# Kernel tuning notes

Measured on AMD Instinct MI355X. Metric: run time of the kernel, lower is better.

The kernel has to match this reference:

```python
import jax, jax.numpy as jnp
import numpy as np

R = 16
LORA_ALPHA = 16.0
SCALING = LORA_ALPHA / R  # = 1.0, matches lora_alpha / r


def setup_inputs() -> dict:
    key = jax.random.key(0)
    k_x, k_a, k_a0, k_b = jax.random.split(key, 4)
    d, r, n_tok = 4096, R, 8192
    inv_sqrt_d = 1.0 / np.sqrt(d)
    x = jax.random.normal(k_x, (n_tok, d), dtype=jnp.float32)
    # mode='standard': A0 ~ N(0, 1/d), B0 = 0; A, B initialized as clones of A0, B0
    A0 = jax.random.normal(k_a0, (r, d), dtype=jnp.float32) * inv_sqrt_d
    B0 = jnp.zeros((d, r), dtype=jnp.float32)
    # perturb A, B slightly to emulate trained params (still faithful math)
    A = A0 + jax.random.normal(k_a, (r, d), dtype=jnp.float32) * inv_sqrt_d
    B = B0 + jax.random.normal(k_b, (d, r), dtype=jnp.float32) * inv_sqrt_d
    return {"x": x, "A": A, "B": B, "A0": A0, "B0": B0}


def reference(x, A, B, A0, B0):
    # Faithful to torch: dW = (B @ A - B0 @ A0) * scaling; out = x @ dW
    # (mode='standard' uses the offset-subtracted delta)
    dW = (B @ A - B0 @ A0) * SCALING          # [d, d]
    return x @ dW                              # [N, d]
```

## Files before the change

### kernel.cpp

```cpp
#include <hip/hip_runtime.h>

#define N_TOK 8192
#define D     4096
#define RLO   16
#define R2    32

typedef __bf16  bf16x8  __attribute__((ext_vector_type(8)));
typedef short   short8v __attribute__((ext_vector_type(8)));
typedef float   f32x4   __attribute__((ext_vector_type(4)));

__device__ __forceinline__ short bf1(float f) {
  __bf16 b = (__bf16)f;
  return __builtin_bit_cast(short, b);
}

__device__ __forceinline__ short8v cvt8(float4 lo, float4 hi) {
  bf16x8 b;
  b[0] = (__bf16)lo.x; b[1] = (__bf16)lo.y; b[2] = (__bf16)lo.z; b[3] = (__bf16)lo.w;
  b[4] = (__bf16)hi.x; b[5] = (__bf16)hi.y; b[6] = (__bf16)hi.z; b[7] = (__bf16)hi.w;
  return __builtin_bit_cast(short8v, b);
}


__global__ __launch_bounds__(256) void prep_kernel(
    const float* __restrict__ A, const float* __restrict__ B,
    const float* __restrict__ A0, const float* __restrict__ B0,
    ushort* __restrict__ PTb, ushort* __restrict__ Qpk) {
  int idx = blockIdx.x * 256 + threadIdx.x;
  int r = idx >> 12;
  int k = idx & (D - 1);
  float pt, q;
  if (r < RLO) {
    pt = B[k * RLO + r];
    q  = A[r * D + k];
  } else {
    pt = -B0[k * RLO + (r - RLO)];
    q  = A0[(r - RLO) * D + k];
  }
  PTb[idx] = (ushort)bf1(pt);
  Qpk[(size_t)k * R2 + r] = (ushort)bf1(q);
}

__global__ __launch_bounds__(256) void fused_kernel(
    const float* __restrict__ x, const ushort* __restrict__ PTb,
    const ushort* __restrict__ Qpk, float* __restrict__ out) {
  __shared__ float red[4][16][R2 + 2];
  __shared__ __align__(16) ushort usb[16][R2];
  const int tid  = threadIdx.x;
  const int w    = tid >> 6;
  const int lane = tid & 63;
  const int l16  = lane & 15;
  const int kg   = lane >> 4;
  const int row0 = blockIdx.x * 16;
  const int kb   = w * 1024 + kg * 8;

  const float*  xp  = x   + (size_t)(row0 + l16) * D + kb;
  const ushort* pb0 = PTb + (size_t)l16 * D + kb;
  const ushort* pb1 = pb0 + (size_t)16 * D;

  f32x4 acc0 = {0.f, 0.f, 0.f, 0.f};
  f32x4 acc1 = {0.f, 0.f, 0.f, 0.f};

#pragma unroll
  for (int s = 0; s < 32; ++s) {
    const int ko = s * 32;
    const float4 alo = *(const float4*)(xp + ko);
    const float4 ahi = *(const float4*)(xp + ko + 4);
    const short8v b0 = *(const short8v*)(pb0 + ko);
    const short8v b1 = *(const short8v*)(pb1 + ko);
    const short8v a  = cvt8(alo, ahi);
    acc0 = __builtin_amdgcn_mfma_f32_16x16x32_bf16(a, b0, acc0, 0, 0, 0);
    acc1 = __builtin_amdgcn_mfma_f32_16x16x32_bf16(a, b1, acc1, 0, 0, 0);
  }

#pragma unroll
  for (int j = 0; j < 4; ++j) {
    red[w][kg * 4 + j][l16]      = acc0[j];
    red[w][kg * 4 + j][16 + l16] = acc1[j];
  }
  __syncthreads();

#pragma unroll
  for (int half = 0; half < 2; ++half) {
    const int idx = half * 256 + tid;
    const int row = idx >> 5;
    const int r   = idx & 31;
    const float s = red[0][row][r] + red[1][row][r] +
                    red[2][row][r] + red[3][row][r];
    usb[row][r] = (ushort)bf1(s);
  }
  __syncthreads();

  const short8v ua = *(const short8v*)&usb[l16][kg * 8];
  const f32x4 z = {0.f, 0.f, 0.f, 0.f};
  const int jbase = w * 1024;

#pragma unroll 8
  for (int jt = 0; jt < 64; ++jt) {
    const int j = jbase + jt * 16 + l16;
    const short8v qb = *(const short8v*)(Qpk + (size_t)j * R2 + kg * 8);
    const f32x4 d = __builtin_amdgcn_mfma_f32_16x16x32_bf16(ua, qb, z, 0, 0, 0);
    float* o = out + (size_t)(row0 + kg * 4) * D + j;
#pragma unroll
    for (int jr = 0; jr < 4; ++jr)
      __builtin_nontemporal_store(d[jr], o + (size_t)jr * D);
  }
}

extern "C" void kernel_launch(void* const* d_in, const int* in_sizes, int n_in,
                              void* d_out, int out_size, void* d_ws, size_t ws_size,
                              hipStream_t stream) {
  const float* x  = (const float*)d_in[0];
  const float* A  = (const float*)d_in[1];
  const float* B  = (const float*)d_in[2];
  const float* A0 = (const float*)d_in[3];
  const float* B0 = (const float*)d_in[4];
  float* out = (float*)d_out;

  ushort* PTb = (ushort*)d_ws;
  ushort* Qpk = PTb + (size_t)R2 * D;

  hipLaunchKernelGGL(prep_kernel, dim3((R2 * D) / 256), dim3(256), 0, stream,
                     A, B, A0, B0, PTb, Qpk);
  hipLaunchKernelGGL(fused_kernel, dim3(N_TOK / 16), dim3(256), 0, stream,
                     x, PTb, Qpk, out);
}
```

Before: 64.38 us.

## Split fused LoRA kernel into split-K projection and separate expansion kernel

Breaks the single fused kernel into two launches. The first computes x·[B,-B0] partial sums with the K dimension split four ways, using four times as many blocks, and writes fp32 partials to workspace. The second sums the partials and runs the rank-32 expansion that writes the output. The aim is to overlap the x read phase and the output write phase across many more blocks, at the cost of an extra launch and a small round trip of the partials through global memory.

New measurement: 93.05 us. 1.45x slower.

```diff
diff --git a/kernel.cpp b/kernel.cpp
--- a/kernel.cpp
+++ b/kernel.cpp
@@ -4,6 +4,7 @@
 #define D     4096
 #define RLO   16
 #define R2    32
+#define KS    4
 
 typedef __bf16  bf16x8  __attribute__((ext_vector_type(8)));
 typedef short   short8v __attribute__((ext_vector_type(8)));
@@ -41,18 +42,19 @@
   Qpk[(size_t)k * R2 + r] = (ushort)bf1(q);
 }
 
-__global__ __launch_bounds__(256) void fused_kernel(
+__global__ __launch_bounds__(256) void s1_kernel(
     const float* __restrict__ x, const ushort* __restrict__ PTb,
-    const ushort* __restrict__ Qpk, float* __restrict__ out) {
+    float* __restrict__ UP) {
   __shared__ float red[4][16][R2 + 2];
-  __shared__ __align__(16) ushort usb[16][R2];
   const int tid  = threadIdx.x;
   const int w    = tid >> 6;
   const int lane = tid & 63;
   const int l16  = lane & 15;
   const int kg   = lane >> 4;
-  const int row0 = blockIdx.x * 16;
-  const int kb   = w * 1024 + kg * 8;
+  const int rowblk = (int)blockIdx.x >> 2;
+  const int ks     = blockIdx.x & 3;
+  const int row0 = rowblk * 16;
+  const int kb   = ks * 1024 + w * 256 + kg * 8;
 
   const float*  xp  = x   + (size_t)(row0 + l16) * D + kb;
   const ushort* pb0 = PTb + (size_t)l16 * D + kb;
@@ -62,7 +64,7 @@
   f32x4 acc1 = {0.f, 0.f, 0.f, 0.f};
 
 #pragma unroll
-  for (int s = 0; s < 32; ++s) {
+  for (int s = 0; s < 8; ++s) {
     const int ko = s * 32;
     const float4 alo = *(const float4*)(xp + ko);
     const float4 ahi = *(const float4*)(xp + ko + 4);
@@ -87,13 +89,42 @@
     const int r   = idx & 31;
     const float s = red[0][row][r] + red[1][row][r] +
                     red[2][row][r] + red[3][row][r];
-    usb[row][r] = (ushort)bf1(s);
+    UP[((size_t)ks * N_TOK + row0 + row) * R2 + r] = s;
+  }
+}
+
+__global__ __launch_bounds__(256) void s2_kernel(
+    const float* __restrict__ UP, const ushort* __restrict__ Qpk,
+    float* __restrict__ out) {
+  __shared__ __align__(16) ushort usb[16][R2];
+  const int tid  = threadIdx.x;
+  const int row0 = (int)blockIdx.x * 16;
+
+  if (tid < 128) {
+    const int row = tid >> 3;
+    const int r4  = (tid & 7) * 4;
+    float4 s = make_float4(0.f, 0.f, 0.f, 0.f);
+#pragma unroll
+    for (int ks = 0; ks < KS; ++ks) {
+      const float4 v =
+          *(const float4*)(UP + ((size_t)ks * N_TOK + row0 + row) * R2 + r4);
+      s.x += v.x; s.y += v.y; s.z += v.z; s.w += v.w;
+    }
+    usb[row][r4 + 0] = (ushort)bf1(s.x);
+    usb[row][r4 + 1] = (ushort)bf1(s.y);
+    usb[row][r4 + 2] = (ushort)bf1(s.z);
+    usb[row][r4 + 3] = (ushort)bf1(s.w);
   }
   __syncthreads();
 
+  const int w    = tid >> 6;
+  const int lane = tid & 63;
+  const int l16  = lane & 15;
+  const int kg   = lane >> 4;
+  const int jbase = w * 1024;
+
   const short8v ua = *(const short8v*)&usb[l16][kg * 8];
   const f32x4 z = {0.f, 0.f, 0.f, 0.f};
-  const int jbase = w * 1024;
 
 #pragma unroll 8
   for (int jt = 0; jt < 64; ++jt) {
@@ -119,9 +150,12 @@
 
   ushort* PTb = (ushort*)d_ws;
   ushort* Qpk = PTb + (size_t)R2 * D;
+  float*  UP  = (float*)(Qpk + (size_t)D * R2);
 
   hipLaunchKernelGGL(prep_kernel, dim3((R2 * D) / 256), dim3(256), 0, stream,
                      A, B, A0, B0, PTb, Qpk);
-  hipLaunchKernelGGL(fused_kernel, dim3(N_TOK / 16), dim3(256), 0, stream,
-                     x, PTb, Qpk, out);
+  hipLaunchKernelGGL(s1_kernel, dim3((N_TOK / 16) * KS), dim3(256), 0, stream,
+                     x, PTb, UP);
+  hipLaunchKernelGGL(s2_kernel, dim3(N_TOK / 16), dim3(256), 0, stream,
+                     UP, Qpk, out);
 }
```
